# Kernel optimization log

Measured on AMD Instinct MI355X. Metric: run time of the kernel, lower is better.

The kernel has to match this reference:

```python
import jax, jax.numpy as jnp
import numpy as np

B, LQ, LKV = 2, 512, 4096
Q_DIM = KV_DIM = QK_OUT = V_OUT = OUT_DIM = 512
H = 8
E = 10
TOPK = 5
QK_HEAD = QK_OUT // H
V_HEAD = V_OUT // H
SCALE = 1.0 / (QK_HEAD ** 0.5)


def _moe_params(key, in_dim, out_dim):
    k1, k2, k3, k4 = jax.random.split(key, 4)
    s = 0.02
    return (
        jax.random.normal(k1, (in_dim, E), dtype=jnp.float32) * s,   # gate W
        jax.random.normal(k2, (E,), dtype=jnp.float32) * s,          # gate b
        jax.random.normal(k3, (E, in_dim, out_dim), dtype=jnp.float32) * s,  # expert W
        jax.random.normal(k4, (E, out_dim), dtype=jnp.float32) * s,  # expert b
    )


def setup_inputs() -> dict:
    key = jax.random.key(0)
    ks = jax.random.split(key, 6)
    q = jax.random.normal(ks[0], (B, LQ, Q_DIM), dtype=jnp.float32)
    kv = jax.random.normal(ks[1], (B, LKV, KV_DIM), dtype=jnp.float32)
    q_gw, q_gb, q_w, q_b = _moe_params(ks[2], Q_DIM, QK_OUT)
    k_gw, k_gb, k_w, k_b = _moe_params(ks[3], KV_DIM, QK_OUT)
    v_gw, v_gb, v_w, v_b = _moe_params(ks[4], KV_DIM, V_OUT)
    o_gw, o_gb, o_w, o_b = _moe_params(ks[5], V_OUT, OUT_DIM)
    return {
        'q': q, 'kv': kv,
        'q_gw': q_gw, 'q_gb': q_gb, 'q_w': q_w, 'q_b': q_b,
        'k_gw': k_gw, 'k_gb': k_gb, 'k_w': k_w, 'k_b': k_b,
        'v_gw': v_gw, 'v_gb': v_gb, 'v_w': v_w, 'v_b': v_b,
        'o_gw': o_gw, 'o_gb': o_gb, 'o_w': o_w, 'o_b': o_b,
    }


def moe_linear(x, gw, gb, W, b, top_k=TOPK):
    # gate: softmax over experts, then keep top-k and renormalize
    gate = jax.nn.softmax(x @ gw + gb, axis=-1)            # [B,S,E]
    topv, idx = jax.lax.top_k(gate, top_k)                 # [B,S,k]
    oneh = jax.nn.one_hot(idx, E, dtype=gate.dtype)        # [B,S,k,E]
    g = jnp.einsum('bsk,bske->bse', topv, oneh)
    g = g / g.sum(-1, keepdims=True)
    # dense compute of all experts, then gate-weighted sum (faithful to source)
    y = jnp.einsum('bsi,eio->bsoe', x, W) + b.T            # [B,S,O,E]
    return jnp.einsum('bsoe,bse->bso', y, g)


def reference(q, kv, q_gw, q_gb, q_w, q_b, k_gw, k_gb, k_w, k_b,
              v_gw, v_gb, v_w, v_b, o_gw, o_gb, o_w, o_b):
    qp = moe_linear(q, q_gw, q_gb, q_w, q_b)               # [B,LQ,QK_OUT]
    kp = moe_linear(kv, k_gw, k_gb, k_w, k_b)              # [B,LKV,QK_OUT]
    vp = moe_linear(kv, v_gw, v_gb, v_w, v_b)              # [B,LKV,V_OUT]
    qh = qp.reshape(B, LQ, H, QK_HEAD).transpose(0, 2, 1, 3)
    kh = kp.reshape(B, LKV, H, QK_HEAD).transpose(0, 2, 1, 3)
    vh = vp.reshape(B, LKV, H, V_HEAD).transpose(0, 2, 1, 3)
    attn = jnp.einsum('bhqd,bhkd->bhqk', qh, kh) * SCALE   # [B,H,LQ,LKV]
    attn = jax.nn.softmax(attn, axis=-1)                   # no mask, dropout=0 (eval)
    x = jnp.einsum('bhqk,bhkd->bhqd', attn, vh)
    x = x.transpose(0, 2, 1, 3).reshape(B, LQ, V_OUT)
    x = moe_linear(x, o_gw, o_gb, o_w, o_b)                # out_proj (also MoE, top_k=5)
    return x, attn
```

## Files before the change

### kernel.cpp

```cpp
#include <hip/hip_runtime.h>
#include <hip/hip_bf16.h>

typedef __bf16 bf16_t;
typedef __bf16 bf16x8 __attribute__((ext_vector_type(8)));
typedef __bf16 bf16x4 __attribute__((ext_vector_type(4)));
typedef float f32x4 __attribute__((ext_vector_type(4)));

#define NE 10
#define DM 512
#define SCALE_F 0.125f

__device__ __forceinline__ void gl16(const void* g, void* l) {
    __builtin_amdgcn_global_load_lds(
        (const __attribute__((address_space(1))) unsigned int*)g,
        (__attribute__((address_space(3))) unsigned int*)l, 16, 0, 0);
}

__global__ void cast_bf16_kernel(const float* __restrict__ in, bf16_t* __restrict__ out, int n)
{
    const int i = (blockIdx.x * 256 + threadIdx.x) * 8;
    if (i >= n) return;
    float4 a = *(const float4*)(in + i);
    float4 b = *(const float4*)(in + i + 4);
    bf16x8 o;
    o[0] = (bf16_t)a.x; o[1] = (bf16_t)a.y; o[2] = (bf16_t)a.z; o[3] = (bf16_t)a.w;
    o[4] = (bf16_t)b.x; o[5] = (bf16_t)b.y; o[6] = (bf16_t)b.z; o[7] = (bf16_t)b.w;
    *(bf16x8*)(out + i) = o;
}

__global__ void wtrans4_kernel(const float* __restrict__ W0, const float* __restrict__ W1,
                               const float* __restrict__ W2, const float* __restrict__ W3,
                               bf16_t* __restrict__ Wt)
{
    __shared__ float tile[32][33];
    const int z = blockIdx.z, which = z / NE, e = z - which * NE;
    const float* W = which == 0 ? W0 : which == 1 ? W1 : which == 2 ? W2 : W3;
    const int n0 = blockIdx.x * 32, k0 = blockIdx.y * 32;
    const int tx = threadIdx.x & 31, ty = threadIdx.x >> 5;
    const float* Wp = W + ((size_t)e * DM + k0) * DM + n0;
#pragma unroll
    for (int r = 0; r < 32; r += 8) tile[ty + r][tx] = Wp[(size_t)(ty + r) * DM + tx];
    __syncthreads();
    bf16_t* Op = Wt + (((size_t)which * NE + e) * DM + n0) * DM + k0;
#pragma unroll
    for (int r = 0; r < 32; r += 8) Op[(size_t)(ty + r) * DM + tx] = (bf16_t)tile[tx][ty + r];
}

__device__ __forceinline__ void topk_write(const float* p, const float* __restrict__ gb,
                                           float* __restrict__ G, int t)
{
    float l[NE], ex[NE];
    float mx = -3.4e38f;
#pragma unroll
    for (int e = 0; e < NE; e++) { l[e] = p[e] + gb[e]; mx = fmaxf(mx, l[e]); }
#pragma unroll
    for (int e = 0; e < NE; e++) ex[e] = __expf(l[e] - mx);
    bool sel[NE];
#pragma unroll
    for (int e = 0; e < NE; e++) sel[e] = false;
    float ssel = 0.f;
    for (int j = 0; j < 5; j++) {
        int bi = 0; float bv = -3.4e38f;
        for (int e = 0; e < NE; e++)
            if (!sel[e] && l[e] > bv) { bv = l[e]; bi = e; }
        sel[bi] = true; ssel += ex[bi];
    }
    const float inv = 1.f / ssel;
    for (int e = 0; e < NE; e++) G[(size_t)t * NE + e] = sel[e] ? ex[e] * inv : 0.f;
}

__global__ void moe_gates(const float* __restrict__ X, const float* __restrict__ gw,
                          const float* __restrict__ gb, float* __restrict__ G)
{
    const int t = blockIdx.x;
    const int lane = threadIdx.x;
    const float* x = X + (size_t)t * DM;
    float p[NE];
#pragma unroll
    for (int e = 0; e < NE; e++) p[e] = 0.f;
    for (int i = lane; i < DM; i += 64) {
        const float xv = x[i];
        const float* g = gw + (size_t)i * NE;
#pragma unroll
        for (int e = 0; e < NE; e++) p[e] += xv * g[e];
    }
#pragma unroll
    for (int off = 32; off > 0; off >>= 1)
#pragma unroll
        for (int e = 0; e < NE; e++) p[e] += __shfl_down(p[e], off);
    if (lane == 0) topk_write(p, gb, G, t);
}

__global__ void moe_gates_kv(const float* __restrict__ X,
                             const float* __restrict__ kgw, const float* __restrict__ kgb,
                             const float* __restrict__ vgw, const float* __restrict__ vgb,
                             float* __restrict__ Gk, float* __restrict__ Gv)
{
    const int t = blockIdx.x * 4 + (threadIdx.x >> 6);
    const int lane = threadIdx.x & 63;
    const float* x = X + (size_t)t * DM;
    float xr[8];
    *(float4*)&xr[0] = *(const float4*)(x + lane * 8);
    *(float4*)&xr[4] = *(const float4*)(x + lane * 8 + 4);
    float pk[NE], pv[NE];
#pragma unroll
    for (int e = 0; e < NE; e++) { pk[e] = 0.f; pv[e] = 0.f; }
#pragma unroll
    for (int j = 0; j < 8; j++) {
        const int i = lane * 8 + j;
        const float* gk = kgw + (size_t)i * NE;
        const float* gv = vgw + (size_t)i * NE;
#pragma unroll
        for (int e = 0; e < NE; e++) { pk[e] += xr[j] * gk[e]; pv[e] += xr[j] * gv[e]; }
    }
#pragma unroll
    for (int off = 32; off > 0; off >>= 1)
#pragma unroll
        for (int e = 0; e < NE; e++) { pk[e] += __shfl_down(pk[e], off); pv[e] += __shfl_down(pv[e], off); }
    if (lane == 0) { topk_write(pk, kgb, Gk, t); topk_write(pv, vgb, Gv, t); }
}

__global__ void gate_bias_init(const float* __restrict__ G, const float* __restrict__ b,
                               float* __restrict__ out)
{
    const int idx = blockIdx.x * 256 + threadIdx.x;
    const int t = idx >> 9, n = idx & 511;
    const float* g = G + (size_t)t * NE;
    float s = 0.f;
#pragma unroll
    for (int e = 0; e < NE; e++) s += g[e] * b[e * DM + n];
    out[idx] = s;
}

__global__ __launch_bounds__(256, 2)
void moe_gemm_kv(const bf16_t* __restrict__ X,
                 const bf16_t* __restrict__ Wk, const bf16_t* __restrict__ Wv,
                 const float* __restrict__ kb, const float* __restrict__ vb,
                 const float* __restrict__ Gk, const float* __restrict__ Gv,
                 bf16_t* __restrict__ kp, bf16_t* __restrict__ vpT)
{
    constexpr int BM = 128, BN = 128, BK = 64;
    __shared__ bf16_t As[BM * BK];
    __shared__ bf16_t Bs[BN * BK];
    __shared__ float Gs[BM][NE];
    __shared__ float BiasS[NE][BN];

    const int tid = threadIdx.x, lane = tid & 63, w = tid >> 6;
    const int wr = w >> 1, wc = w & 1;
    const int l15 = lane & 15, quad = lane >> 4;
    const int m0 = blockIdx.x * BM;
    const int side = blockIdx.y >> 2;
    const int n0 = (blockIdx.y & 3) * BN;
    const bf16_t* Wt = side ? Wv : Wk;
    const float* G = side ? Gv : Gk;
    const float* bias = side ? vb : kb;

    for (int i = tid; i < BM * NE; i += 256) {
        int r = i / NE, e = i - r * NE;
        Gs[r][e] = G[(size_t)(m0 + r) * NE + e];
    }
    for (int i = tid; i < NE * BN; i += 256) {
        int e = i / BN, j = i - e * BN;
        BiasS[e][j] = bias[(size_t)e * DM + n0 + j];
    }

    const int rsub = lane >> 3, pch = lane & 7, csw = pch ^ rsub;
    const bf16_t* aptr[4]; bf16_t* alds[4]; bf16_t* blds[4];
#pragma unroll
    for (int j = 0; j < 4; j++) {
        const int rb = w * 32 + j * 8;
        aptr[j] = X + (size_t)(m0 + rb + rsub) * DM + csw * 8;
        alds[j] = (bf16_t*)As + rb * BK;
        blds[j] = (bf16_t*)Bs + rb * BK;
    }
    int amr[4], bnr[4];
#pragma unroll
    for (int f = 0; f < 4; f++) { amr[f] = wr * 64 + f * 16 + l15; bnr[f] = wc * 64 + f * 16 + l15; }

    const f32x4 zv = {0.f, 0.f, 0.f, 0.f};
    f32x4 acc[4][4];
#pragma unroll
    for (int a = 0; a < 4; a++)
#pragma unroll
        for (int c = 0; c < 4; c++) acc[a][c] = zv;

    for (int e = 0; e < NE; e++) {
        const bf16_t* bbase = Wt + ((size_t)e * DM + n0 + w * 32 + rsub) * DM + csw * 8;
        f32x4 acc2[4][4];
#pragma unroll
        for (int a = 0; a < 4; a++)
#pragma unroll
            for (int c = 0; c < 4; c++) acc2[a][c] = zv;

        for (int kt = 0; kt < 8; kt++) {
            __syncthreads();
#pragma unroll
            for (int j = 0; j < 4; j++) gl16(aptr[j] + kt * BK, alds[j]);
#pragma unroll
            for (int j = 0; j < 4; j++) gl16(bbase + (size_t)j * 8 * DM + kt * BK, blds[j]);
            __syncthreads();
#pragma unroll
            for (int kss = 0; kss < 2; kss++) {
                bf16x8 af[4], bf[4];
#pragma unroll
                for (int f = 0; f < 4; f++) {
                    af[f] = *(const bf16x8*)(As + amr[f] * BK + (((kss << 2) | quad) ^ (amr[f] & 7)) * 8);
                    bf[f] = *(const bf16x8*)(Bs + bnr[f] * BK + (((kss << 2) | quad) ^ (bnr[f] & 7)) * 8);
                }
#pragma unroll
                for (int mf = 0; mf < 4; mf++)
#pragma unroll
                    for (int nf = 0; nf < 4; nf++)
                        acc2[mf][nf] = __builtin_amdgcn_mfma_f32_16x16x32_bf16(
                            af[mf], bf[nf], acc2[mf][nf], 0, 0, 0);
            }
        }
#pragma unroll
        for (int mf = 0; mf < 4; mf++)
#pragma unroll
            for (int r = 0; r < 4; r++) {
                const float g = Gs[wr * 64 + mf * 16 + quad * 4 + r][e];
#pragma unroll
                for (int nf = 0; nf < 4; nf++) acc[mf][nf][r] += g * acc2[mf][nf][r];
            }
    }

#pragma unroll
    for (int mf = 0; mf < 4; mf++) {
#pragma unroll
        for (int nf = 0; nf < 4; nf++) {
            const int n = wc * 64 + nf * 16 + l15;
            float vals[4];
#pragma unroll
            for (int r = 0; r < 4; r++) {
                const int m = wr * 64 + mf * 16 + quad * 4 + r;
                float v = acc[mf][nf][r];
#pragma unroll
                for (int e = 0; e < NE; e++) v += Gs[m][e] * BiasS[e][n];
                vals[r] = v;
            }
            if (side) {
                const int mg = m0 + wr * 64 + mf * 16 + quad * 4;
                const int b = mg >> 12, t = mg & 4095;
                bf16x4 pk;
                pk[0] = (bf16_t)vals[0]; pk[1] = (bf16_t)vals[1];
                pk[2] = (bf16_t)vals[2]; pk[3] = (bf16_t)vals[3];
                *(bf16x4*)(vpT + ((size_t)(b * DM) + n0 + n) * 4096 + t) = pk;
            } else {
#pragma unroll
                for (int r = 0; r < 4; r++) {
                    const int m = wr * 64 + mf * 16 + quad * 4 + r;
                    kp[(size_t)(m0 + m) * DM + n0 + n] = (bf16_t)vals[r];
                }
            }
        }
    }
}

__global__ __launch_bounds__(256, 4)
void moe_gemm_split(const bf16_t* __restrict__ X, const bf16_t* __restrict__ Wt,
                    const float* __restrict__ G, float* __restrict__ out)
{
    constexpr int BK = 64;
    __shared__ bf16_t As[64 * BK];
    __shared__ bf16_t Bs[64 * BK];
    __shared__ float Gs[64][2];
    const int tid = threadIdx.x, lane = tid & 63, w = tid >> 6;
    const int wr = w >> 1, wc = w & 1;
    const int l15 = lane & 15, quad = lane >> 4;
    const int m0 = blockIdx.x * 64, n0 = blockIdx.y * 64, e0 = blockIdx.z * 2;

    if (tid < 128) {
        int r = tid >> 1, e = tid & 1;
        Gs[r][e] = G[(size_t)(m0 + r) * NE + e0 + e];
    }

    const int rsub = lane >> 3, pch = lane & 7, csw = pch ^ rsub;
    const bf16_t* aptr[2]; bf16_t* alds[2]; bf16_t* blds[2];
#pragma unroll
    for (int j = 0; j < 2; j++) {
        const int rb = w * 16 + j * 8;
        aptr[j] = X + (size_t)(m0 + rb + rsub) * DM + csw * 8;
        alds[j] = (bf16_t*)As + rb * BK;
        blds[j] = (bf16_t*)Bs + rb * BK;
    }
    const int amr[2] = {wr * 32 + l15, wr * 32 + 16 + l15};
    const int bnr[2] = {wc * 32 + l15, wc * 32 + 16 + l15};

    const f32x4 zv = {0.f, 0.f, 0.f, 0.f};
    f32x4 acc[2][2];
#pragma unroll
    for (int a = 0; a < 2; a++)
#pragma unroll
        for (int c = 0; c < 2; c++) acc[a][c] = zv;

#pragma unroll
    for (int ee = 0; ee < 2; ee++) {
        const int e = e0 + ee;
        const bf16_t* bbase = Wt + ((size_t)e * DM + n0 + w * 16 + rsub) * DM + csw * 8;
        f32x4 acc2[2][2];
#pragma unroll
        for (int a = 0; a < 2; a++)
#pragma unroll
            for (int c = 0; c < 2; c++) acc2[a][c] = zv;
        for (int kt = 0; kt < 8; kt++) {
            __syncthreads();
#pragma unroll
            for (int j = 0; j < 2; j++) gl16(aptr[j] + kt * BK, alds[j]);
#pragma unroll
            for (int j = 0; j < 2; j++) gl16(bbase + (size_t)j * 8 * DM + kt * BK, blds[j]);
            __syncthreads();
#pragma unroll
            for (int kss = 0; kss < 2; kss++) {
                bf16x8 af[2], bf[2];
#pragma unroll
                for (int f = 0; f < 2; f++) {
                    af[f] = *(const bf16x8*)(As + amr[f] * BK + (((kss << 2) | quad) ^ (amr[f] & 7)) * 8);
                    bf[f] = *(const bf16x8*)(Bs + bnr[f] * BK + (((kss << 2) | quad) ^ (bnr[f] & 7)) * 8);
                }
#pragma unroll
                for (int mf = 0; mf < 2; mf++)
#pragma unroll
                    for (int nf = 0; nf < 2; nf++)
                        acc2[mf][nf] = __builtin_amdgcn_mfma_f32_16x16x32_bf16(
                            af[mf], bf[nf], acc2[mf][nf], 0, 0, 0);
            }
        }
#pragma unroll
        for (int mf = 0; mf < 2; mf++)
#pragma unroll
            for (int r = 0; r < 4; r++) {
                const float g = Gs[wr * 32 + mf * 16 + quad * 4 + r][ee];
#pragma unroll
                for (int nf = 0; nf < 2; nf++) acc[mf][nf][r] += g * acc2[mf][nf][r];
            }
    }
#pragma unroll
    for (int mf = 0; mf < 2; mf++)
#pragma unroll
        for (int nf = 0; nf < 2; nf++) {
            const int n = n0 + wc * 32 + nf * 16 + l15;
#pragma unroll
            for (int r = 0; r < 4; r++) {
                const int m = m0 + wr * 32 + mf * 16 + quad * 4 + r;
                atomicAdd(&out[(size_t)m * DM + n], acc[mf][nf][r]);
            }
        }
}

__global__ __launch_bounds__(256, 2)
void attn_pass1(const float* __restrict__ qp, const bf16_t* __restrict__ kp,
                float* __restrict__ mws, float* __restrict__ lws)
{
    __shared__ bf16_t Qs[64][72];
    __shared__ bf16_t Ks[64 * 64];
    const int ksp = blockIdx.x, qt = blockIdx.y, bh = blockIdx.z;
    const int b = bh >> 3, h = bh & 7, q0 = qt * 64;
    const int tid = threadIdx.x, lane = tid & 63, w = tid >> 6;
    const int l15 = lane & 15, quad = lane >> 4;

    {
        const int row = tid >> 2, cg = (tid & 3) * 16;
        const float* qs = qp + ((size_t)(b * 512 + q0 + row)) * DM + h * 64 + cg;
        float4 f[4];
#pragma unroll
        for (int j = 0; j < 4; j++) f[j] = *(const float4*)(qs + j * 4);
        bf16x8 o0, o1;
        o0[0]=(bf16_t)(f[0].x*SCALE_F); o0[1]=(bf16_t)(f[0].y*SCALE_F); o0[2]=(bf16_t)(f[0].z*SCALE_F); o0[3]=(bf16_t)(f[0].w*SCALE_F);
        o0[4]=(bf16_t)(f[1].x*SCALE_F); o0[5]=(bf16_t)(f[1].y*SCALE_F); o0[6]=(bf16_t)(f[1].z*SCALE_F); o0[7]=(bf16_t)(f[1].w*SCALE_F);
        o1[0]=(bf16_t)(f[2].x*SCALE_F); o1[1]=(bf16_t)(f[2].y*SCALE_F); o1[2]=(bf16_t)(f[2].z*SCALE_F); o1[3]=(bf16_t)(f[2].w*SCALE_F);
        o1[4]=(bf16_t)(f[3].x*SCALE_F); o1[5]=(bf16_t)(f[3].y*SCALE_F); o1[6]=(bf16_t)(f[3].z*SCALE_F); o1[7]=(bf16_t)(f[3].w*SCALE_F);
        *(bf16x8*)&Qs[row][cg] = o0;
        *(bf16x8*)&Qs[row][cg + 8] = o1;
    }
    const int rsub = lane >> 3, pch = lane & 7, csw = pch ^ rsub;
    const bf16_t* kptr[2]; bf16_t* klds[2];
#pragma unroll
    for (int j = 0; j < 2; j++) {
        const int rb = w * 16 + j * 8;
        kptr[j] = kp + ((size_t)(b * 4096 + rb + rsub)) * DM + h * 64 + csw * 8;
        klds[j] = (bf16_t*)Ks + rb * 64;
    }
    float mrun[4], lrun[4];
#pragma unroll
    for (int r = 0; r < 4; r++) { mrun[r] = -3.0e38f; lrun[r] = 0.f; }

    for (int kt = 0; kt < 16; kt++) {
        const size_t koff = (size_t)(ksp * 16 + kt) * 64 * DM;
        __syncthreads();
        gl16(kptr[0] + koff, klds[0]);
        gl16(kptr[1] + koff, klds[1]);
        __syncthreads();
        const f32x4 zv = {0.f, 0.f, 0.f, 0.f};
        f32x4 sacc[4] = {zv, zv, zv, zv};
#pragma unroll
        for (int kss = 0; kss < 2; kss++) {
            bf16x8 af = *(const bf16x8*)&Qs[w * 16 + l15][kss * 32 + quad * 8];
#pragma unroll
            for (int nf = 0; nf < 4; nf++) {
                const int br = nf * 16 + l15;
                bf16x8 bf = *(const bf16x8*)(Ks + br * 64 + (((kss << 2) | quad) ^ (br & 7)) * 8);
                sacc[nf] = __builtin_amdgcn_mfma_f32_16x16x32_bf16(af, bf, sacc[nf], 0, 0, 0);
            }
        }
#pragma unroll
        for (int r = 0; r < 4; r++) {
            float tm = fmaxf(fmaxf(sacc[0][r], sacc[1][r]), fmaxf(sacc[2][r], sacc[3][r]));
#pragma unroll
            for (int off = 1; off < 16; off <<= 1) tm = fmaxf(tm, __shfl_xor(tm, off));
            const float mn = fmaxf(mrun[r], tm);
            float s = __expf(sacc[0][r] - mn) + __expf(sacc[1][r] - mn) +
                      __expf(sacc[2][r] - mn) + __expf(sacc[3][r] - mn);
#pragma unroll
            for (int off = 1; off < 16; off <<= 1) s += __shfl_xor(s, off);
            lrun[r] = lrun[r] * __expf(mrun[r] - mn) + s;
            mrun[r] = mn;
        }
    }
    if (l15 == 0) {
#pragma unroll
        for (int r = 0; r < 4; r++) {
            const int row = q0 + w * 16 + quad * 4 + r;
            mws[((size_t)ksp * 16 + bh) * 512 + row] = mrun[r];
            lws[((size_t)ksp * 16 + bh) * 512 + row] = lrun[r];
        }
    }
}

__global__ __launch_bounds__(256, 2)
void attn_pass2(const float* __restrict__ qp, const bf16_t* __restrict__ kp,
                const bf16_t* __restrict__ vpT, const float* __restrict__ mws,
                const float* __restrict__ lws, float* __restrict__ attn,
                float* __restrict__ xout)
{
    __shared__ bf16_t Qs[64][72];
    __shared__ bf16_t Ks[64 * 64];
    __shared__ bf16_t Vs[64 * 64];
    __shared__ bf16_t Ps[64][72];
    const int ksp = blockIdx.x, qt = blockIdx.y, bh = blockIdx.z;
    const int b = bh >> 3, h = bh & 7, q0 = qt * 64;
    const int tid = threadIdx.x, lane = tid & 63, w = tid >> 6;
    const int l15 = lane & 15, quad = lane >> 4;

    {
        const int row = tid >> 2, cg = (tid & 3) * 16;
        const float* qs = qp + ((size_t)(b * 512 + q0 + row)) * DM + h * 64 + cg;
        float4 f[4];
#pragma unroll
        for (int j = 0; j < 4; j++) f[j] = *(const float4*)(qs + j * 4);
        bf16x8 o0, o1;
        o0[0]=(bf16_t)(f[0].x*SCALE_F); o0[1]=(bf16_t)(f[0].y*SCALE_F); o0[2]=(bf16_t)(f[0].z*SCALE_F); o0[3]=(bf16_t)(f[0].w*SCALE_F);
        o0[4]=(bf16_t)(f[1].x*SCALE_F); o0[5]=(bf16_t)(f[1].y*SCALE_F); o0[6]=(bf16_t)(f[1].z*SCALE_F); o0[7]=(bf16_t)(f[1].w*SCALE_F);
        o1[0]=(bf16_t)(f[2].x*SCALE_F); o1[1]=(bf16_t)(f[2].y*SCALE_F); o1[2]=(bf16_t)(f[2].z*SCALE_F); o1[3]=(bf16_t)(f[2].w*SCALE_F);
        o1[4]=(bf16_t)(f[3].x*SCALE_F); o1[5]=(bf16_t)(f[3].y*SCALE_F); o1[6]=(bf16_t)(f[3].z*SCALE_F); o1[7]=(bf16_t)(f[3].w*SCALE_F);
        *(bf16x8*)&Qs[row][cg] = o0;
        *(bf16x8*)&Qs[row][cg + 8] = o1;
    }
    float mrow[4], linv[4];
#pragma unroll
    for (int r = 0; r < 4; r++) {
        const int row = q0 + w * 16 + quad * 4 + r;
        float mv[4], lv[4], mm = -3.0e38f;
#pragma unroll
        for (int p = 0; p < 4; p++) {
            mv[p] = mws[((size_t)p * 16 + bh) * 512 + row];
            lv[p] = lws[((size_t)p * 16 + bh) * 512 + row];
            mm = fmaxf(mm, mv[p]);
        }
        float ll = 0.f;
#pragma unroll
        for (int p = 0; p < 4; p++) ll += lv[p] * __expf(mv[p] - mm);
        mrow[r] = mm; linv[r] = 1.f / ll;
    }
    const int rsub = lane >> 3, pch = lane & 7, csw = pch ^ rsub;
    const bf16_t* kptr[2]; const bf16_t* vptr[2]; bf16_t* klds[2]; bf16_t* vlds[2];
#pragma unroll
    for (int j = 0; j < 2; j++) {
        const int rb = w * 16 + j * 8;
        kptr[j] = kp + ((size_t)(b * 4096 + rb + rsub)) * DM + h * 64 + csw * 8;
        vptr[j] = vpT + ((size_t)(b * DM + h * 64 + rb + rsub)) * 4096 + csw * 8;
        klds[j] = (bf16_t*)Ks + rb * 64;
        vlds[j] = (bf16_t*)Vs + rb * 64;
    }
    const f32x4 zv = {0.f, 0.f, 0.f, 0.f};
    f32x4 oacc[4] = {zv, zv, zv, zv};
    float* ap = attn + ((size_t)bh * 512) * 4096;

    for (int kt = 0; kt < 16; kt++) {
        const int kg = (ksp * 16 + kt) * 64;
        __syncthreads();
        gl16(kptr[0] + (size_t)kg * DM, klds[0]);
        gl16(kptr[1] + (size_t)kg * DM, klds[1]);
        gl16(vptr[0] + kg, vlds[0]);
        gl16(vptr[1] + kg, vlds[1]);
        __syncthreads();
        f32x4 sacc[4] = {zv, zv, zv, zv};
#pragma unroll
        for (int kss = 0; kss < 2; kss++) {
            bf16x8 af = *(const bf16x8*)&Qs[w * 16 + l15][kss * 32 + quad * 8];
#pragma unroll
            for (int nf = 0; nf < 4; nf++) {
                const int br = nf * 16 + l15;
                bf16x8 bf = *(const bf16x8*)(Ks + br * 64 + (((kss << 2) | quad) ^ (br & 7)) * 8);
                sacc[nf] = __builtin_amdgcn_mfma_f32_16x16x32_bf16(af, bf, sacc[nf], 0, 0, 0);
            }
        }
#pragma unroll
        for (int nf = 0; nf < 4; nf++)
#pragma unroll
            for (int r = 0; r < 4; r++) {
                const float p = __expf(sacc[nf][r] - mrow[r]) * linv[r];
                ap[((size_t)(q0 + w * 16 + quad * 4 + r)) * 4096 + kg + nf * 16 + l15] = p;
                Ps[w * 16 + quad * 4 + r][nf * 16 + l15] = (bf16_t)p;
            }
        __syncthreads();
#pragma unroll
        for (int kss = 0; kss < 2; kss++) {
            bf16x8 paf = *(const bf16x8*)&Ps[w * 16 + l15][kss * 32 + quad * 8];
#pragma unroll
            for (int nf = 0; nf < 4; nf++) {
                const int br = nf * 16 + l15;
                bf16x8 vb = *(const bf16x8*)(Vs + br * 64 + (((kss << 2) | quad) ^ (br & 7)) * 8);
                oacc[nf] = __builtin_amdgcn_mfma_f32_16x16x32_bf16(paf, vb, oacc[nf], 0, 0, 0);
            }
        }
    }
#pragma unroll
    for (int nf = 0; nf < 4; nf++) {
        const int n = h * 64 + nf * 16 + l15;
#pragma unroll
        for (int r = 0; r < 4; r++) {
            const int m = b * 512 + q0 + w * 16 + quad * 4 + r;
            atomicAdd(&xout[(size_t)m * DM + n], oacc[nf][r]);
        }
    }
}

extern "C" void kernel_launch(void* const* d_in, const int* in_sizes, int n_in,
                              void* d_out, int out_size, void* d_ws, size_t ws_size,
                              hipStream_t stream)
{
    (void)in_sizes; (void)n_in; (void)out_size; (void)ws_size;
    const float* q    = (const float*)d_in[0];
    const float* kv   = (const float*)d_in[1];
    const float* q_gw = (const float*)d_in[2];
    const float* q_gb = (const float*)d_in[3];
    const float* q_w  = (const float*)d_in[4];
    const float* q_b  = (const float*)d_in[5];
    const float* k_gw = (const float*)d_in[6];
    const float* k_gb = (const float*)d_in[7];
    const float* k_w  = (const float*)d_in[8];
    const float* k_b  = (const float*)d_in[9];
    const float* v_gw = (const float*)d_in[10];
    const float* v_gb = (const float*)d_in[11];
    const float* v_w  = (const float*)d_in[12];
    const float* v_b  = (const float*)d_in[13];
    const float* o_gw = (const float*)d_in[14];
    const float* o_gb = (const float*)d_in[15];
    const float* o_w  = (const float*)d_in[16];
    const float* o_b  = (const float*)d_in[17];

    float* out0 = (float*)d_out;
    float* attn = out0 + (size_t)1024 * 512;

    char* ws = (char*)d_ws;
    size_t off = 0;
    auto alloc = [&](size_t bytes) {
        void* p = ws + off;
        off += (bytes + 255) & ~(size_t)255;
        return p;
    };
    bf16_t* Xq    = (bf16_t*)alloc((size_t)1024 * 512 * 2);
    bf16_t* Xkv   = (bf16_t*)alloc((size_t)8192 * 512 * 2);
    bf16_t* Wall  = (bf16_t*)alloc((size_t)4 * NE * 512 * 512 * 2);
    bf16_t* Wq_t  = Wall;
    bf16_t* Wk_t  = Wall + (size_t)1 * NE * 512 * 512;
    bf16_t* Wv_t  = Wall + (size_t)2 * NE * 512 * 512;
    bf16_t* Wo_t  = Wall + (size_t)3 * NE * 512 * 512;
    float*  qpf   = (float*)alloc((size_t)1024 * 512 * 4);
    bf16_t* kp    = (bf16_t*)alloc((size_t)8192 * 512 * 2);
    bf16_t* vpT   = (bf16_t*)alloc((size_t)8192 * 512 * 2);
    float*  xatt  = (float*)alloc((size_t)1024 * 512 * 4);
    bf16_t* xbf   = (bf16_t*)alloc((size_t)1024 * 512 * 2);
    float*  Gq    = (float*)alloc((size_t)1024 * NE * 4);
    float*  Gk    = (float*)alloc((size_t)8192 * NE * 4);
    float*  Gv    = (float*)alloc((size_t)8192 * NE * 4);
    float*  Go    = (float*)alloc((size_t)1024 * NE * 4);
    float*  mws   = (float*)alloc((size_t)4 * 16 * 512 * 4);
    float*  lws   = (float*)alloc((size_t)4 * 16 * 512 * 4);

    cast_bf16_kernel<<<256, 256, 0, stream>>>(q, Xq, 1024 * 512);
    cast_bf16_kernel<<<2048, 256, 0, stream>>>(kv, Xkv, 8192 * 512);
    wtrans4_kernel<<<dim3(16, 16, 4 * NE), 256, 0, stream>>>(q_w, k_w, v_w, o_w, Wall);
    moe_gates<<<1024, 64, 0, stream>>>(q, q_gw, q_gb, Gq);
    moe_gates_kv<<<2048, 256, 0, stream>>>(kv, k_gw, k_gb, v_gw, v_gb, Gk, Gv);

    gate_bias_init<<<2048, 256, 0, stream>>>(Gq, q_b, qpf);
    moe_gemm_split<<<dim3(16, 8, 5), 256, 0, stream>>>(Xq, Wq_t, Gq, qpf);
    moe_gemm_kv<<<dim3(64, 8), 256, 0, stream>>>(Xkv, Wk_t, Wv_t, k_b, v_b, Gk, Gv, kp, vpT);

    attn_pass1<<<dim3(4, 8, 16), 256, 0, stream>>>(qpf, kp, mws, lws);
    hipMemsetAsync(xatt, 0, (size_t)1024 * 512 * 4, stream);
    attn_pass2<<<dim3(4, 8, 16), 256, 0, stream>>>(qpf, kp, vpT, mws, lws, attn, xatt);

    moe_gates<<<1024, 64, 0, stream>>>(xatt, o_gw, o_gb, Go);
    cast_bf16_kernel<<<256, 256, 0, stream>>>(xatt, xbf, 1024 * 512);
    gate_bias_init<<<2048, 256, 0, stream>>>(Go, o_b, out0);
    moe_gemm_split<<<dim3(16, 8, 5), 256, 0, stream>>>(xbf, Wo_t, Go, out0);
}
```

Measured before the change: 465.2 us.

## Double-buffer LDS tiles in MoE GEMMs and attention kernels to overlap loads

Result: slower. 521.4 us (+12.1%).

```diff
diff --git a/kernel.cpp b/kernel.cpp
--- a/kernel.cpp
+++ b/kernel.cpp
@@ -140,8 +140,8 @@
                  bf16_t* __restrict__ kp, bf16_t* __restrict__ vpT)
 {
     constexpr int BM = 128, BN = 128, BK = 64;
-    __shared__ bf16_t As[BM * BK];
-    __shared__ bf16_t Bs[BN * BK];
+    __shared__ bf16_t As[2][BM * BK];
+    __shared__ bf16_t Bs[2][BN * BK];
     __shared__ float Gs[BM][NE];
     __shared__ float BiasS[NE][BN];
 
@@ -165,17 +165,26 @@
     }
 
     const int rsub = lane >> 3, pch = lane & 7, csw = pch ^ rsub;
-    const bf16_t* aptr[4]; bf16_t* alds[4]; bf16_t* blds[4];
+    const bf16_t* aptr[4]; int soff[4];
 #pragma unroll
     for (int j = 0; j < 4; j++) {
         const int rb = w * 32 + j * 8;
         aptr[j] = X + (size_t)(m0 + rb + rsub) * DM + csw * 8;
-        alds[j] = (bf16_t*)As + rb * BK;
-        blds[j] = (bf16_t*)Bs + rb * BK;
-    }
+        soff[j] = rb * BK;
+    }
+    const bf16_t* wb0 = Wt + ((size_t)(n0 + w * 32 + rsub)) * DM + csw * 8;
     int amr[4], bnr[4];
 #pragma unroll
     for (int f = 0; f < 4; f++) { amr[f] = wr * 64 + f * 16 + l15; bnr[f] = wc * 64 + f * 16 + l15; }
+
+    auto stage = [&](int buf, int it) {
+        const int e_ = it >> 3, kt_ = it & 7;
+        const bf16_t* bb = wb0 + (size_t)e_ * (DM * DM) + kt_ * BK;
+#pragma unroll
+        for (int j = 0; j < 4; j++) gl16(aptr[j] + kt_ * BK, &As[buf][soff[j]]);
+#pragma unroll
+        for (int j = 0; j < 4; j++) gl16(bb + (size_t)j * 8 * DM, &Bs[buf][soff[j]]);
+    };
 
     const f32x4 zv = {0.f, 0.f, 0.f, 0.f};
     f32x4 acc[4][4];
@@ -184,8 +193,11 @@
 #pragma unroll
         for (int c = 0; c < 4; c++) acc[a][c] = zv;
 
+    stage(0, 0);
+    __syncthreads();
+    int cur = 0;
+
     for (int e = 0; e < NE; e++) {
-        const bf16_t* bbase = Wt + ((size_t)e * DM + n0 + w * 32 + rsub) * DM + csw * 8;
         f32x4 acc2[4][4];
 #pragma unroll
         for (int a = 0; a < 4; a++)
@@ -193,27 +205,25 @@
             for (int c = 0; c < 4; c++) acc2[a][c] = zv;
 
         for (int kt = 0; kt < 8; kt++) {
-            __syncthreads();
-#pragma unroll
-            for (int j = 0; j < 4; j++) gl16(aptr[j] + kt * BK, alds[j]);
-#pragma unroll
-            for (int j = 0; j < 4; j++) gl16(bbase + (size_t)j * 8 * DM + kt * BK, blds[j]);
-            __syncthreads();
+            const int itn = e * 8 + kt + 1;
+            if (itn < NE * 8) stage(cur ^ 1, itn);
 #pragma unroll
             for (int kss = 0; kss < 2; kss++) {
-                bf16x8 af[4], bf[4];
+                bf16x8 af[4], bfr[4];
 #pragma unroll
                 for (int f = 0; f < 4; f++) {
-                    af[f] = *(const bf16x8*)(As + amr[f] * BK + (((kss << 2) | quad) ^ (amr[f] & 7)) * 8);
-                    bf[f] = *(const bf16x8*)(Bs + bnr[f] * BK + (((kss << 2) | quad) ^ (bnr[f] & 7)) * 8);
+                    af[f]  = *(const bf16x8*)(&As[cur][amr[f] * BK + (((kss << 2) | quad) ^ (amr[f] & 7)) * 8]);
+                    bfr[f] = *(const bf16x8*)(&Bs[cur][bnr[f] * BK + (((kss << 2) | quad) ^ (bnr[f] & 7)) * 8]);
                 }
 #pragma unroll
                 for (int mf = 0; mf < 4; mf++)
 #pragma unroll
                     for (int nf = 0; nf < 4; nf++)
                         acc2[mf][nf] = __builtin_amdgcn_mfma_f32_16x16x32_bf16(
-                            af[mf], bf[nf], acc2[mf][nf], 0, 0, 0);
-            }
+                            af[mf], bfr[nf], acc2[mf][nf], 0, 0, 0);
+            }
+            __syncthreads();
+            cur ^= 1;
         }
 #pragma unroll
         for (int mf = 0; mf < 4; mf++)
@@ -262,8 +272,8 @@
                     const float* __restrict__ G, float* __restrict__ out)
 {
     constexpr int BK = 64;
-    __shared__ bf16_t As[64 * BK];
-    __shared__ bf16_t Bs[64 * BK];
+    __shared__ bf16_t As[2][64 * BK];
+    __shared__ bf16_t Bs[2][64 * BK];
     __shared__ float Gs[64][2];
     const int tid = threadIdx.x, lane = tid & 63, w = tid >> 6;
     const int wr = w >> 1, wc = w & 1;
@@ -276,17 +286,26 @@
     }
 
     const int rsub = lane >> 3, pch = lane & 7, csw = pch ^ rsub;
-    const bf16_t* aptr[2]; bf16_t* alds[2]; bf16_t* blds[2];
+    const bf16_t* aptr[2]; int soff[2];
 #pragma unroll
     for (int j = 0; j < 2; j++) {
         const int rb = w * 16 + j * 8;
         aptr[j] = X + (size_t)(m0 + rb + rsub) * DM + csw * 8;
-        alds[j] = (bf16_t*)As + rb * BK;
-        blds[j] = (bf16_t*)Bs + rb * BK;
-    }
+        soff[j] = rb * BK;
+    }
+    const bf16_t* wb0 = Wt + ((size_t)(n0 + w * 16 + rsub)) * DM + csw * 8;
     const int amr[2] = {wr * 32 + l15, wr * 32 + 16 + l15};
     const int bnr[2] = {wc * 32 + l15, wc * 32 + 16 + l15};
 
+    auto stage = [&](int buf, int it) {
+        const int e_ = e0 + (it >> 3), kt_ = it & 7;
+        const bf16_t* bb = wb0 + (size_t)e_ * (DM * DM) + kt_ * BK;
+#pragma unroll
+        for (int j = 0; j < 2; j++) gl16(aptr[j] + kt_ * BK, &As[buf][soff[j]]);
+#pragma unroll
+        for (int j = 0; j < 2; j++) gl16(bb + (size_t)j * 8 * DM, &Bs[buf][soff[j]]);
+    };
+
     const f32x4 zv = {0.f, 0.f, 0.f, 0.f};
     f32x4 acc[2][2];
 #pragma unroll
@@ -294,37 +313,37 @@
 #pragma unroll
         for (int c = 0; c < 2; c++) acc[a][c] = zv;
 
+    stage(0, 0);
+    __syncthreads();
+    int cur = 0;
+
 #pragma unroll
     for (int ee = 0; ee < 2; ee++) {
-        const int e = e0 + ee;
-        const bf16_t* bbase = Wt + ((size_t)e * DM + n0 + w * 16 + rsub) * DM + csw * 8;
         f32x4 acc2[2][2];
 #pragma unroll
         for (int a = 0; a < 2; a++)
 #pragma unroll
             for (int c = 0; c < 2; c++) acc2[a][c] = zv;
         for (int kt = 0; kt < 8; kt++) {
-            __syncthreads();
-#pragma unroll
-            for (int j = 0; j < 2; j++) gl16(aptr[j] + kt * BK, alds[j]);
-#pragma unroll
-            for (int j = 0; j < 2; j++) gl16(bbase + (size_t)j * 8 * DM + kt * BK, blds[j]);
-            __syncthreads();
+            const int itn = ee * 8 + kt + 1;
+            if (itn < 16) stage(cur ^ 1, itn);
 #pragma unroll
             for (int kss = 0; kss < 2; kss++) {
-                bf16x8 af[2], bf[2];
+                bf16x8 af[2], bfr[2];
 #pragma unroll
                 for (int f = 0; f < 2; f++) {
-                    af[f] = *(const bf16x8*)(As + amr[f] * BK + (((kss << 2) | quad) ^ (amr[f] & 7)) * 8);
-                    bf[f] = *(const bf16x8*)(Bs + bnr[f] * BK + (((kss << 2) | quad) ^ (bnr[f] & 7)) * 8);
+                    af[f]  = *(const bf16x8*)(&As[cur][amr[f] * BK + (((kss << 2) | quad) ^ (amr[f] & 7)) * 8]);
+                    bfr[f] = *(const bf16x8*)(&Bs[cur][bnr[f] * BK + (((kss << 2) | quad) ^ (bnr[f] & 7)) * 8]);
                 }
 #pragma unroll
                 for (int mf = 0; mf < 2; mf++)
 #pragma unroll
                     for (int nf = 0; nf < 2; nf++)
                         acc2[mf][nf] = __builtin_amdgcn_mfma_f32_16x16x32_bf16(
-                            af[mf], bf[nf], acc2[mf][nf], 0, 0, 0);
-            }
+                            af[mf], bfr[nf], acc2[mf][nf], 0, 0, 0);
+            }
+            __syncthreads();
+            cur ^= 1;
         }
 #pragma unroll
         for (int mf = 0; mf < 2; mf++)
@@ -353,7 +372,7 @@
                 float* __restrict__ mws, float* __restrict__ lws)
 {
     __shared__ bf16_t Qs[64][72];
-    __shared__ bf16_t Ks[64 * 64];
+    __shared__ bf16_t Ks[2][64 * 64];
     const int ksp = blockIdx.x, qt = blockIdx.y, bh = blockIdx.z;
     const int b = bh >> 3, h = bh & 7, q0 = qt * 64;
     const int tid = threadIdx.x, lane = tid & 63, w = tid >> 6;
@@ -374,23 +393,31 @@
         *(bf16x8*)&Qs[row][cg + 8] = o1;
     }
     const int rsub = lane >> 3, pch = lane & 7, csw = pch ^ rsub;
-    const bf16_t* kptr[2]; bf16_t* klds[2];
+    const bf16_t* kptr[2]; int loff[2];
 #pragma unroll
     for (int j = 0; j < 2; j++) {
         const int rb = w * 16 + j * 8;
         kptr[j] = kp + ((size_t)(b * 4096 + rb + rsub)) * DM + h * 64 + csw * 8;
-        klds[j] = (bf16_t*)Ks + rb * 64;
+        loff[j] = rb * 64;
     }
     float mrun[4], lrun[4];
 #pragma unroll
     for (int r = 0; r < 4; r++) { mrun[r] = -3.0e38f; lrun[r] = 0.f; }
 
+    {
+        const size_t koff = (size_t)(ksp * 16) * 64 * DM;
+        gl16(kptr[0] + koff, &Ks[0][loff[0]]);
+        gl16(kptr[1] + koff, &Ks[0][loff[1]]);
+    }
+    __syncthreads();
+    int cur = 0;
+
     for (int kt = 0; kt < 16; kt++) {
-        const size_t koff = (size_t)(ksp * 16 + kt) * 64 * DM;
-        __syncthreads();
-        gl16(kptr[0] + koff, klds[0]);
-        gl16(kptr[1] + koff, klds[1]);
-        __syncthreads();
+        if (kt < 15) {
+            const size_t koff = (size_t)(ksp * 16 + kt + 1) * 64 * DM;
+            gl16(kptr[0] + koff, &Ks[cur ^ 1][loff[0]]);
+            gl16(kptr[1] + koff, &Ks[cur ^ 1][loff[1]]);
+        }
         const f32x4 zv = {0.f, 0.f, 0.f, 0.f};
         f32x4 sacc[4] = {zv, zv, zv, zv};
 #pragma unroll
@@ -399,8 +426,8 @@
 #pragma unroll
             for (int nf = 0; nf < 4; nf++) {
                 const int br = nf * 16 + l15;
-                bf16x8 bf = *(const bf16x8*)(Ks + br * 64 + (((kss << 2) | quad) ^ (br & 7)) * 8);
-                sacc[nf] = __builtin_amdgcn_mfma_f32_16x16x32_bf16(af, bf, sacc[nf], 0, 0, 0);
+                bf16x8 bfr = *(const bf16x8*)(&Ks[cur][br * 64 + (((kss << 2) | quad) ^ (br & 7)) * 8]);
+                sacc[nf] = __builtin_amdgcn_mfma_f32_16x16x32_bf16(af, bfr, sacc[nf], 0, 0, 0);
             }
         }
 #pragma unroll
@@ -416,6 +443,8 @@
             lrun[r] = lrun[r] * __expf(mrun[r] - mn) + s;
             mrun[r] = mn;
         }
+        __syncthreads();
+        cur ^= 1;
     }
     if (l15 == 0) {
 #pragma unroll
@@ -434,8 +463,8 @@
                 float* __restrict__ xout)
 {
     __shared__ bf16_t Qs[64][72];
-    __shared__ bf16_t Ks[64 * 64];
-    __shared__ bf16_t Vs[64 * 64];
+    __shared__ bf16_t Ks[2][64 * 64];
+    __shared__ bf16_t Vs[2][64 * 64];
     __shared__ bf16_t Ps[64][72];
     const int ksp = blockIdx.x, qt = blockIdx.y, bh = blockIdx.z;
     const int b = bh >> 3, h = bh & 7, q0 = qt * 64;
@@ -473,27 +502,37 @@
         mrow[r] = mm; linv[r] = 1.f / ll;
     }
     const int rsub = lane >> 3, pch = lane & 7, csw = pch ^ rsub;
-    const bf16_t* kptr[2]; const bf16_t* vptr[2]; bf16_t* klds[2]; bf16_t* vlds[2];
+    const bf16_t* kptr[2]; const bf16_t* vptr[2]; int loff[2];
 #pragma unroll
     for (int j = 0; j < 2; j++) {
         const int rb = w * 16 + j * 8;
         kptr[j] = kp + ((size_t)(b * 4096 + rb + rsub)) * DM + h * 64 + csw * 8;
         vptr[j] = vpT + ((size_t)(b * DM + h * 64 + rb + rsub)) * 4096 + csw * 8;
-        klds[j] = (bf16_t*)Ks + rb * 64;
-        vlds[j] = (bf16_t*)Vs + rb * 64;
+        loff[j] = rb * 64;
     }
     const f32x4 zv = {0.f, 0.f, 0.f, 0.f};
     f32x4 oacc[4] = {zv, zv, zv, zv};
     float* ap = attn + ((size_t)bh * 512) * 4096;
 
+    {
+        const int kg0 = (ksp * 16) * 64;
+        gl16(kptr[0] + (size_t)kg0 * DM, &Ks[0][loff[0]]);
+        gl16(kptr[1] + (size_t)kg0 * DM, &Ks[0][loff[1]]);
+        gl16(vptr[0] + kg0, &Vs[0][loff[0]]);
+        gl16(vptr[1] + kg0, &Vs[0][loff[1]]);
+    }
+    __syncthreads();
+    int cur = 0;
+
     for (int kt = 0; kt < 16; kt++) {
         const int kg = (ksp * 16 + kt) * 64;
-        __syncthreads();
-        gl16(kptr[0] + (size_t)kg * DM, klds[0]);
-        gl16(kptr[1] + (size_t)kg * DM, klds[1]);
-        gl16(vptr[0] + kg, vlds[0]);
-        gl16(vptr[1] + kg, vlds[1]);
-        __syncthreads();
+        if (kt < 15) {
+            const int kgn = kg + 64;
+            gl16(kptr[0] + (size_t)kgn * DM, &Ks[cur ^ 1][loff[0]]);
+            gl16(kptr[1] + (size_t)kgn * DM, &Ks[cur ^ 1][loff[1]]);
+            gl16(vptr[0] + kgn, &Vs[cur ^ 1][loff[0]]);
+            gl16(vptr[1] + kgn, &Vs[cur ^ 1][loff[1]]);
+        }
         f32x4 sacc[4] = {zv, zv, zv, zv};
 #pragma unroll
         for (int kss = 0; kss < 2; kss++) {
@@ -501,8 +540,8 @@
 #pragma unroll
             for (int nf = 0; nf < 4; nf++) {
                 const int br = nf * 16 + l15;
-                bf16x8 bf = *(const bf16x8*)(Ks + br * 64 + (((kss << 2) | quad) ^ (br & 7)) * 8);
-                sacc[nf] = __builtin_amdgcn_mfma_f32_16x16x32_bf16(af, bf, sacc[nf], 0, 0, 0);
+                bf16x8 bfr = *(const bf16x8*)(&Ks[cur][br * 64 + (((kss << 2) | quad) ^ (br & 7)) * 8]);
+                sacc[nf] = __builtin_amdgcn_mfma_f32_16x16x32_bf16(af, bfr, sacc[nf], 0, 0, 0);
             }
         }
 #pragma unroll
@@ -520,10 +559,12 @@
 #pragma unroll
             for (int nf = 0; nf < 4; nf++) {
                 const int br = nf * 16 + l15;
-                bf16x8 vb = *(const bf16x8*)(Vs + br * 64 + (((kss << 2) | quad) ^ (br & 7)) * 8);
+                bf16x8 vb = *(const bf16x8*)(&Vs[cur][br * 64 + (((kss << 2) | quad) ^ (br & 7)) * 8]);
                 oacc[nf] = __builtin_amdgcn_mfma_f32_16x16x32_bf16(paf, vb, oacc[nf], 0, 0, 0);
             }
         }
+        __syncthreads();
+        cur ^= 1;
     }
 #pragma unroll
     for (int nf = 0; nf < 4; nf++) {
```
